# Optimization experiments

Hardware: AMD Instinct MI355X
Metric: run time of the kernel (lower is better)

## Reference

```python
import jax, jax.numpy as jnp
import numpy as np

D_MODEL = 1024
NUM_HEADS = 16
HEAD_DIM = D_MODEL // NUM_HEADS  # 64
THETA = 10000.0
B, S = 2, 2048


def setup_inputs() -> dict:
    key = jax.random.key(0)
    k1, k2, k3 = jax.random.split(key, 3)
    sigma_qkv = (2.0 / (D_MODEL + 3 * D_MODEL)) ** 0.5
    sigma_o = (2.0 / (D_MODEL + D_MODEL)) ** 0.5
    x = jax.random.normal(k1, (B, S, D_MODEL), dtype=jnp.float32)
    w_qkv = jax.random.normal(k2, (3 * D_MODEL, D_MODEL), dtype=jnp.float32) * sigma_qkv
    w_o = jax.random.normal(k3, (D_MODEL, D_MODEL), dtype=jnp.float32) * sigma_o
    token_positions = jnp.arange(S, dtype=jnp.int32)
    return {"x": x, "w_qkv": w_qkv, "w_o": w_o, "token_positions": token_positions, "mask": 1}


def _rope(t, pos):
    # t: (B, H, S, HEAD_DIM); pos: (S,) int
    ids = jnp.arange(HEAD_DIM // 2, dtype=jnp.float32)
    freqs = pos.astype(jnp.float32)[:, None] * (THETA ** (-2.0 * ids / HEAD_DIM))  # (S, HEAD_DIM/2)
    cos, sin = jnp.cos(freqs), jnp.sin(freqs)
    even, odd = t[..., 0::2], t[..., 1::2]
    r_even = even * cos - odd * sin
    r_odd = odd * cos + even * sin
    # interleave back to original layout
    return jnp.stack([r_even, r_odd], axis=-1).reshape(t.shape)


def reference(x, w_qkv, w_o, token_positions, mask):
    # fused QKV projection: Linear computes x @ W^T with W [out, in]
    qkv = x @ w_qkv.T  # (B, S, 3*D_MODEL)
    q, k, v = jnp.split(qkv, 3, axis=-1)

    def to_heads(t):
        return t.reshape(B, S, NUM_HEADS, HEAD_DIM).transpose(0, 2, 1, 3)  # (B, H, S, Dh)

    q, k, v = to_heads(q), to_heads(k), to_heads(v)
    q = _rope(q, token_positions)
    k = _rope(k, token_positions)

    scores = jnp.einsum('bhqd,bhkd->bhqk', q, k)
    if mask:  # causal: lower-triangular allowed
        causal = jnp.tril(jnp.ones((S, S), dtype=bool))
        scores = jnp.where(causal, scores, -jnp.inf)
    attn = jax.nn.softmax(scores * (HEAD_DIM ** -0.5), axis=-1)
    out = jnp.einsum('bhqk,bhkd->bhqd', attn, v)  # (B, H, S, Dh)
    out = out.transpose(0, 2, 1, 3).reshape(B, S, D_MODEL)
    return out @ w_o.T
```

## Files before the change

kernel.cpp:

```cpp
#include <hip/hip_runtime.h>
#include <hip/hip_bf16.h>
#include <math.h>

typedef __bf16 bf16_t;
typedef __bf16 bf16x8 __attribute__((ext_vector_type(8)));
typedef __bf16 bf16x4 __attribute__((ext_vector_type(4)));
typedef float  f32x4  __attribute__((ext_vector_type(4)));
typedef float  f32x16 __attribute__((ext_vector_type(16)));

#define D_MODEL 1024
#define NH      16
#define HD      64
#define BATCH   2
#define SEQ     2048
#define MROWS   (BATCH*SEQ)
#define QKVN    (3*D_MODEL)
#define FA_PAD  72
#define PADK    40
#define SCALE_LOG2E 0.18033688011112042f

__device__ __forceinline__ void async_cp16(const bf16_t* g, bf16_t* l) {
    __builtin_amdgcn_global_load_lds(
        (const __attribute__((address_space(1))) void*)g,
        (__attribute__((address_space(3))) void*)l,
        16, 0, 0);
}

__device__ __forceinline__ float fexp2(float x) {
    float r;
    asm("v_exp_f32 %0, %1" : "=v"(r) : "v"(x));
    return r;
}

__global__ void cvt_all(const float* __restrict__ x, const float* __restrict__ wq,
                        const float* __restrict__ wo,
                        bf16_t* __restrict__ xb, bf16_t* __restrict__ wqb,
                        bf16_t* __restrict__ wob) {
    const int nx = MROWS * D_MODEL, nq = QKVN * D_MODEL;
    int i = (blockIdx.x * blockDim.x + threadIdx.x) * 4;
    const float* s; bf16_t* d; int off;
    if (i < nx)           { s = x;  d = xb;  off = i; }
    else if (i < nx + nq) { s = wq; d = wqb; off = i - nx; }
    else                  { s = wo; d = wob; off = i - nx - nq; }
    float4 v = *(const float4*)(s + off);
    d[off]     = (bf16_t)v.x;
    d[off + 1] = (bf16_t)v.y;
    d[off + 2] = (bf16_t)v.z;
    d[off + 3] = (bf16_t)v.w;
}

template <typename OutT, int NI>
__global__ __launch_bounds__(256) void gemm_nt(const bf16_t* __restrict__ A,
                                               const bf16_t* __restrict__ Bm,
                                               OutT* __restrict__ C,
                                               int M, int N, int K) {
    __shared__ __align__(16) bf16_t As[128 * 32];
    __shared__ __align__(16) bf16_t Bs[NI * 32 * 32];
    const int tid  = threadIdx.x;
    const int w    = tid >> 6;
    const int lane = tid & 63;
    const int quad = lane >> 4;
    const int l16  = lane & 15;
    const int m0   = blockIdx.x * 128;
    const int n0   = blockIdx.y * (NI * 32);
    const int wm   = (w >> 1) * 64;
    const int wn   = (w & 1) * (NI * 16);

    f32x4 acc[4][NI];
    #pragma unroll
    for (int i = 0; i < 4; i++)
        #pragma unroll
        for (int j = 0; j < NI; j++)
            acc[i][j] = (f32x4){0.f, 0.f, 0.f, 0.f};

    const bf16_t* Ag0 = A  + (size_t)(m0 + (tid >> 2)) * K + (tid & 3) * 8;
    const bf16_t* Ag1 = Ag0 + (size_t)64 * K;
    const bf16_t* Bg0 = Bm + (size_t)(n0 + (tid >> 2)) * K + (tid & 3) * 8;
    const bf16_t* Bg1 = Bg0 + (size_t)64 * K;
    bf16_t* Al0 = &As[(size_t)tid * 8];
    bf16_t* Al1 = &As[((size_t)tid + 256) * 8];
    bf16_t* Bl0 = &Bs[(size_t)tid * 8];
    bf16_t* Bl1 = &Bs[((size_t)tid + 256) * 8];

    for (int k0 = 0; k0 < K; k0 += 32) {
        async_cp16(Ag0 + k0, Al0);
        async_cp16(Ag1 + k0, Al1);
        async_cp16(Bg0 + k0, Bl0);
        if (NI == 4) async_cp16(Bg1 + k0, Bl1);
        __syncthreads();

        bf16x8 af[4], bfr[NI];
        #pragma unroll
        for (int mi = 0; mi < 4; mi++)
            af[mi] = *(const bf16x8*)&As[(wm + mi * 16 + l16) * 32 + quad * 8];
        #pragma unroll
        for (int ni = 0; ni < NI; ni++)
            bfr[ni] = *(const bf16x8*)&Bs[(wn + ni * 16 + l16) * 32 + quad * 8];
        #pragma unroll
        for (int mi = 0; mi < 4; mi++)
            #pragma unroll
            for (int ni = 0; ni < NI; ni++)
                acc[mi][ni] = __builtin_amdgcn_mfma_f32_16x16x32_bf16(
                    af[mi], bfr[ni], acc[mi][ni], 0, 0, 0);
        __syncthreads();
    }

    #pragma unroll
    for (int mi = 0; mi < 4; mi++)
        #pragma unroll
        for (int ni = 0; ni < NI; ni++) {
            const int col = n0 + wn + ni * 16 + l16;
            #pragma unroll
            for (int r = 0; r < 4; r++) {
                const int row = m0 + wm + mi * 16 + quad * 4 + r;
                C[(size_t)row * N + col] = (OutT)acc[mi][ni][r];
            }
        }
}

__global__ __launch_bounds__(256) void rope_split(const bf16_t* __restrict__ qkv,
                                                  const int* __restrict__ pos,
                                                  bf16_t* __restrict__ Qh,
                                                  bf16_t* __restrict__ Kh,
                                                  bf16_t* __restrict__ VT) {
    __shared__ bf16_t vs[128][FA_PAD];
    const int tid   = threadIdx.x;
    const int s_loc = tid >> 1;
    const int half  = tid & 1;
    const int s0    = blockIdx.x * 128;
    const int bh    = blockIdx.y;
    const int b     = bh >> 4, h = bh & 15;
    const int s     = s0 + s_loc;

    const bf16_t* row = qkv + (size_t)(b * SEQ + s) * QKVN + h * HD + half * 32;

    bf16_t qbuf[32], kbuf[32], vbuf[32];
    #pragma unroll
    for (int j = 0; j < 4; j++) {
        *(bf16x8*)&qbuf[j * 8] = *(const bf16x8*)(row + j * 8);
        *(bf16x8*)&kbuf[j * 8] = *(const bf16x8*)(row + D_MODEL + j * 8);
        *(bf16x8*)&vbuf[j * 8] = *(const bf16x8*)(row + 2 * D_MODEL + j * 8);
    }

    const float pf = (float)pos[s];
    #pragma unroll
    for (int p = 0; p < 16; p++) {
        const int d2 = half * 16 + p;
        const float inv = __expf(-0.28782313662425575f * (float)d2);
        const float f = pf * inv;
        const float c = cosf(f), sn = sinf(f);
        float qe = (float)qbuf[2 * p], qo = (float)qbuf[2 * p + 1];
        float ke = (float)kbuf[2 * p], ko = (float)kbuf[2 * p + 1];
        qbuf[2 * p]     = (bf16_t)(qe * c - qo * sn);
        qbuf[2 * p + 1] = (bf16_t)(qo * c + qe * sn);
        kbuf[2 * p]     = (bf16_t)(ke * c - ko * sn);
        kbuf[2 * p + 1] = (bf16_t)(ko * c + ke * sn);
    }

    bf16_t* qdst = Qh + ((size_t)bh * SEQ + s) * HD + half * 32;
    bf16_t* kdst = Kh + ((size_t)bh * SEQ + s) * HD + half * 32;
    #pragma unroll
    for (int j = 0; j < 4; j++) {
        *(bf16x8*)(qdst + j * 8) = *(bf16x8*)&qbuf[j * 8];
        *(bf16x8*)(kdst + j * 8) = *(bf16x8*)&kbuf[j * 8];
        *(bf16x8*)&vs[s_loc][half * 32 + j * 8] = *(bf16x8*)&vbuf[j * 8];
    }
    __syncthreads();

    const int d  = tid >> 2;
    const int sc = tid & 3;
    bf16_t tmp[32];
    #pragma unroll
    for (int i = 0; i < 32; i++) tmp[i] = vs[sc * 32 + i][d];
    bf16_t* vdst = VT + ((size_t)bh * HD + d) * SEQ + s0 + sc * 32;
    #pragma unroll
    for (int j = 0; j < 4; j++)
        *(bf16x8*)(vdst + j * 8) = *(bf16x8*)&tmp[j * 8];
}

__global__ __launch_bounds__(256) void flash_attn(const bf16_t* __restrict__ Qh,
                                                  const bf16_t* __restrict__ Kh,
                                                  const bf16_t* __restrict__ VT,
                                                  bf16_t* __restrict__ AO) {
    __shared__ __align__(16) char smem[64 * FA_PAD * 2 * 2 + 4 * 32 * PADK * 2];
    bf16_t* Ks = (bf16_t*)smem;
    bf16_t* Vs = Ks + 64 * FA_PAD;
    bf16_t* pT = Vs + 64 * FA_PAD;

    const int tid  = threadIdx.x;
    const int w    = tid >> 6;
    const int lane = tid & 63;
    const int l31  = lane & 31;
    const int hi   = lane >> 5;
    const int qh   = w & 1;
    const int kh   = w >> 1;

    const int bid  = blockIdx.x;
    const int bh   = bid & 31;
    const int my_t = 31 - (bid >> 5);
    const int nkv  = my_t + 1;

    const bf16_t* Qb = Qh + (size_t)bh * SEQ * HD;
    const bf16_t* Kb = Kh + (size_t)bh * SEQ * HD;
    const bf16_t* Vb = VT + (size_t)bh * HD * SEQ;

    const int q0b = my_t * 64;
    const int qlo = q0b + qh * 32;
    const int qg  = qlo + l31;

    bf16x8 aq[4];
    #pragma unroll
    for (int ks = 0; ks < 4; ks++)
        aq[ks] = *(const bf16x8*)(Qb + (size_t)qg * HD + ks * 16 + hi * 8);

    const int srow = tid >> 3, scol = (tid & 7) * 8;
    const int lds0 = srow * FA_PAD + scol;
    const int lds1 = (srow + 32) * FA_PAD + scol;

    f32x16 o[2];
    #pragma unroll
    for (int dt = 0; dt < 2; dt++)
        #pragma unroll
        for (int i = 0; i < 16; i++) o[dt][i] = 0.f;
    float ls = 0.f;

    bf16x8 pK0 = *(const bf16x8*)(Kb + (size_t)srow * HD + scol);
    bf16x8 pK1 = *(const bf16x8*)(Kb + (size_t)(srow + 32) * HD + scol);
    bf16x8 pV0 = *(const bf16x8*)(Vb + (size_t)srow * SEQ + scol);
    bf16x8 pV1 = *(const bf16x8*)(Vb + (size_t)(srow + 32) * SEQ + scol);

    bf16_t* pb = &pT[(w * 32 + l31) * PADK];

    for (int kt = 0; kt < nkv; ++kt) {
        *(bf16x8*)&Ks[lds0] = pK0;
        *(bf16x8*)&Ks[lds1] = pK1;
        *(bf16x8*)&Vs[lds0] = pV0;
        *(bf16x8*)&Vs[lds1] = pV1;
        __syncthreads();

        if (kt + 1 < nkv) {
            const int kn = (kt + 1) * 64;
            pK0 = *(const bf16x8*)(Kb + (size_t)(kn + srow) * HD + scol);
            pK1 = *(const bf16x8*)(Kb + (size_t)(kn + srow + 32) * HD + scol);
            pV0 = *(const bf16x8*)(Vb + (size_t)srow * SEQ + kn + scol);
            pV1 = *(const bf16x8*)(Vb + (size_t)(srow + 32) * SEQ + kn + scol);
        }

        const int kvbw = kt * 64 + kh * 32;
        if (kvbw <= qlo + 31) {
            const bool full = (kvbw + 31 <= qlo);

            bf16x8 kb[4];
            #pragma unroll
            for (int ks = 0; ks < 4; ks++)
                kb[ks] = *(const bf16x8*)&Ks[(kh * 32 + l31) * FA_PAD + ks * 16 + hi * 8];
            f32x16 t;
            #pragma unroll
            for (int i = 0; i < 16; i++) t[i] = 0.f;
            #pragma unroll
            for (int ks = 0; ks < 4; ks++)
                t = __builtin_amdgcn_mfma_f32_32x32x16_bf16(kb[ks], aq[ks], t, 0, 0, 0);

            bf16x4 pk[4];
            #pragma unroll
            for (int r = 0; r < 16; r++) {
                float pv = fexp2(t[r] * SCALE_LOG2E);
                if (!full) {
                    const int kvg = kvbw + (r & 3) + 8 * (r >> 2) + 4 * hi;
                    if (kvg > qg) pv = 0.f;
                }
                ls += pv;
                pk[r >> 2][r & 3] = (bf16_t)pv;
            }
            #pragma unroll
            for (int g = 0; g < 4; g++)
                *(bf16x4*)&pb[8 * g + 4 * hi] = pk[g];

            bf16x8 pa0 = *(const bf16x8*)&pb[hi * 8];
            bf16x8 pa1 = *(const bf16x8*)&pb[16 + hi * 8];
            #pragma unroll
            for (int dt = 0; dt < 2; dt++) {
                const int vbase = (dt * 32 + l31) * FA_PAD + kh * 32 + hi * 8;
                bf16x8 vf0 = *(const bf16x8*)&Vs[vbase];
                bf16x8 vf1 = *(const bf16x8*)&Vs[vbase + 16];
                o[dt] = __builtin_amdgcn_mfma_f32_32x32x16_bf16(pa0, vf0, o[dt], 0, 0, 0);
                o[dt] = __builtin_amdgcn_mfma_f32_32x32x16_bf16(pa1, vf1, o[dt], 0, 0, 0);
            }
        }

        __syncthreads();
    }

    ls += __shfl_xor(ls, 32);
    float* mrgO = (float*)smem;
    float* lsp  = mrgO + 2 * 32 * 66;
    if (kh == 1) {
        #pragma unroll
        for (int r = 0; r < 16; r++) {
            const int qlc = (r & 3) + 8 * (r >> 2) + 4 * hi;
            #pragma unroll
            for (int dt = 0; dt < 2; dt++)
                mrgO[(qh * 32 + qlc) * 66 + dt * 32 + l31] = o[dt][r];
        }
        if (hi == 0) lsp[qh * 32 + l31] = ls;
    }
    __syncthreads();
    if (kh == 0) {
        const float lt = ls + lsp[qh * 32 + l31];
        const int b = bh >> 4, hh = bh & 15;
        #pragma unroll
        for (int r = 0; r < 16; r++) {
            const int qlc = (r & 3) + 8 * (r >> 2) + 4 * hi;
            const float li = 1.0f / __shfl(lt, qlc);
            const size_t row = (size_t)b * SEQ + q0b + qh * 32 + qlc;
            #pragma unroll
            for (int dt = 0; dt < 2; dt++) {
                const float v = o[dt][r] + mrgO[(qh * 32 + qlc) * 66 + dt * 32 + l31];
                AO[row * D_MODEL + hh * HD + dt * 32 + l31] = (bf16_t)(v * li);
            }
        }
    }
}

extern "C" void kernel_launch(void* const* d_in, const int* in_sizes, int n_in,
                              void* d_out, int out_size, void* d_ws, size_t ws_size,
                              hipStream_t stream) {
    const float* x     = (const float*)d_in[0];
    const float* w_qkv = (const float*)d_in[1];
    const float* w_o   = (const float*)d_in[2];
    const int*   tpos  = (const int*)d_in[3];
    float*       out   = (float*)d_out;

    char* ws = (char*)d_ws;
    bf16_t* xb  = (bf16_t*)(ws);
    bf16_t* wqb = (bf16_t*)(ws + 8388608);
    bf16_t* wob = (bf16_t*)(ws + 14680064);
    bf16_t* qkv = (bf16_t*)(ws + 16777216);
    bf16_t* Qh  = (bf16_t*)(ws + 41943040);
    bf16_t* Kh  = (bf16_t*)(ws + 50331648);
    bf16_t* VT  = (bf16_t*)(ws + 58720256);
    bf16_t* AO  = (bf16_t*)(ws + 67108864);

    cvt_all<<<8192, 256, 0, stream>>>(x, w_qkv, w_o, xb, wqb, wob);

    gemm_nt<bf16_t, 4><<<dim3(32, 24), 256, 0, stream>>>(xb, wqb, qkv, MROWS, QKVN, D_MODEL);

    rope_split<<<dim3(SEQ / 128, BATCH * NH), 256, 0, stream>>>(qkv, tpos, Qh, Kh, VT);

    flash_attn<<<1024, 256, 0, stream>>>(Qh, Kh, VT, AO);

    gemm_nt<float, 2><<<dim3(32, 16), 256, 0, stream>>>(AO, wob, out, MROWS, D_MODEL, D_MODEL);
}
```

Measured before the change: 193.8 us.

## Double-buffer K/V in LDS, keep P in registers via permlane swap, prescale Q

The flash attention kernel now uses two LDS buffers for K and V. Each iteration stores the next tile into the alternate buffer after compute, so one barrier per iteration replaces two. The probability tile no longer round-trips through LDS: it is packed with v_cvt_pk_bf16_f32 and rearranged with v_permlane32_swap into the MFMA A-operand layout in registers. The softmax scale times log2e is folded into Q during the RoPE pass, which removes a multiply per score but rounds the scaled Q to bf16.

```diff
diff --git a/kernel.cpp b/kernel.cpp
--- a/kernel.cpp
+++ b/kernel.cpp
@@ -16,7 +16,6 @@
 #define MROWS   (BATCH*SEQ)
 #define QKVN    (3*D_MODEL)
 #define FA_PAD  72
-#define PADK    40
 #define SCALE_LOG2E 0.18033688011112042f
 
 __device__ __forceinline__ void async_cp16(const bf16_t* g, bf16_t* l) {
@@ -29,6 +28,12 @@
 __device__ __forceinline__ float fexp2(float x) {
     float r;
     asm("v_exp_f32 %0, %1" : "=v"(r) : "v"(x));
+    return r;
+}
+
+__device__ __forceinline__ unsigned cvtpk(float lo, float hi_) {
+    unsigned r;
+    asm("v_cvt_pk_bf16_f32 %0, %1, %2" : "=v"(r) : "v"(lo), "v"(hi_));
     return r;
 }
 
@@ -151,8 +156,8 @@
         const float c = cosf(f), sn = sinf(f);
         float qe = (float)qbuf[2 * p], qo = (float)qbuf[2 * p + 1];
         float ke = (float)kbuf[2 * p], ko = (float)kbuf[2 * p + 1];
-        qbuf[2 * p]     = (bf16_t)(qe * c - qo * sn);
-        qbuf[2 * p + 1] = (bf16_t)(qo * c + qe * sn);
+        qbuf[2 * p]     = (bf16_t)((qe * c - qo * sn) * SCALE_LOG2E);
+        qbuf[2 * p + 1] = (bf16_t)((qo * c + qe * sn) * SCALE_LOG2E);
         kbuf[2 * p]     = (bf16_t)(ke * c - ko * sn);
         kbuf[2 * p + 1] = (bf16_t)(ko * c + ke * sn);
     }
@@ -182,10 +187,10 @@
                                                   const bf16_t* __restrict__ Kh,
                                                   const bf16_t* __restrict__ VT,
                                                   bf16_t* __restrict__ AO) {
-    __shared__ __align__(16) char smem[64 * FA_PAD * 2 * 2 + 4 * 32 * PADK * 2];
-    bf16_t* Ks = (bf16_t*)smem;
-    bf16_t* Vs = Ks + 64 * FA_PAD;
-    bf16_t* pT = Vs + 64 * FA_PAD;
+    __shared__ __align__(16) bf16_t smem[4 * 64 * FA_PAD];
+    bf16_t* Ks0 = smem;
+    bf16_t* Vs0 = smem + 2 * 64 * FA_PAD;
+    const int BUF = 64 * FA_PAD;
 
     const int tid  = threadIdx.x;
     const int w    = tid >> 6;
@@ -228,14 +233,13 @@
     bf16x8 pK1 = *(const bf16x8*)(Kb + (size_t)(srow + 32) * HD + scol);
     bf16x8 pV0 = *(const bf16x8*)(Vb + (size_t)srow * SEQ + scol);
     bf16x8 pV1 = *(const bf16x8*)(Vb + (size_t)(srow + 32) * SEQ + scol);
-
-    bf16_t* pb = &pT[(w * 32 + l31) * PADK];
+    *(bf16x8*)&Ks0[lds0] = pK0;
+    *(bf16x8*)&Ks0[lds1] = pK1;
+    *(bf16x8*)&Vs0[lds0] = pV0;
+    *(bf16x8*)&Vs0[lds1] = pV1;
 
     for (int kt = 0; kt < nkv; ++kt) {
-        *(bf16x8*)&Ks[lds0] = pK0;
-        *(bf16x8*)&Ks[lds1] = pK1;
-        *(bf16x8*)&Vs[lds0] = pV0;
-        *(bf16x8*)&Vs[lds1] = pV1;
+        const int cur = kt & 1;
         __syncthreads();
 
         if (kt + 1 < nkv) {
@@ -246,6 +250,8 @@
             pV1 = *(const bf16x8*)(Vb + (size_t)(srow + 32) * SEQ + kn + scol);
         }
 
+        const bf16_t* KsC = Ks0 + cur * BUF;
+        const bf16_t* VsC = Vs0 + cur * BUF;
         const int kvbw = kt * 64 + kh * 32;
         if (kvbw <= qlo + 31) {
             const bool full = (kvbw + 31 <= qlo);
@@ -253,7 +259,7 @@
             bf16x8 kb[4];
             #pragma unroll
             for (int ks = 0; ks < 4; ks++)
-                kb[ks] = *(const bf16x8*)&Ks[(kh * 32 + l31) * FA_PAD + ks * 16 + hi * 8];
+                kb[ks] = *(const bf16x8*)&KsC[(kh * 32 + l31) * FA_PAD + ks * 16 + hi * 8];
             f32x16 t;
             #pragma unroll
             for (int i = 0; i < 16; i++) t[i] = 0.f;
@@ -261,36 +267,62 @@
             for (int ks = 0; ks < 4; ks++)
                 t = __builtin_amdgcn_mfma_f32_32x32x16_bf16(kb[ks], aq[ks], t, 0, 0, 0);
 
-            bf16x4 pk[4];
+            float pv[16];
             #pragma unroll
             for (int r = 0; r < 16; r++) {
-                float pv = fexp2(t[r] * SCALE_LOG2E);
+                float p = fexp2(t[r]);
                 if (!full) {
                     const int kvg = kvbw + (r & 3) + 8 * (r >> 2) + 4 * hi;
-                    if (kvg > qg) pv = 0.f;
+                    if (kvg > qg) p = 0.f;
                 }
-                ls += pv;
-                pk[r >> 2][r & 3] = (bf16_t)pv;
-            }
-            #pragma unroll
-            for (int g = 0; g < 4; g++)
-                *(bf16x4*)&pb[8 * g + 4 * hi] = pk[g];
-
-            bf16x8 pa0 = *(const bf16x8*)&pb[hi * 8];
-            bf16x8 pa1 = *(const bf16x8*)&pb[16 + hi * 8];
+                pv[r] = p;
+            }
+            ls += ((((pv[0] + pv[1]) + (pv[2] + pv[3]))
+                  + ((pv[4] + pv[5]) + (pv[6] + pv[7])))
+                 + (((pv[8] + pv[9]) + (pv[10] + pv[11]))
+                  + ((pv[12] + pv[13]) + (pv[14] + pv[15]))));
+
+            union { unsigned u[4]; bf16x8 v; } pa0, pa1;
+            {
+                unsigned a0 = cvtpk(pv[0], pv[1]);
+                unsigned b0 = cvtpk(pv[4], pv[5]);
+                unsigned a1 = cvtpk(pv[2], pv[3]);
+                unsigned b1 = cvtpk(pv[6], pv[7]);
+                asm volatile("v_permlane32_swap_b32 %0, %1" : "+v"(a0), "+v"(b0));
+                asm volatile("v_permlane32_swap_b32 %0, %1" : "+v"(a1), "+v"(b1));
+                pa0.u[0] = a0; pa0.u[1] = a1; pa0.u[2] = b0; pa0.u[3] = b1;
+            }
+            {
+                unsigned a0 = cvtpk(pv[8], pv[9]);
+                unsigned b0 = cvtpk(pv[12], pv[13]);
+                unsigned a1 = cvtpk(pv[10], pv[11]);
+                unsigned b1 = cvtpk(pv[14], pv[15]);
+                asm volatile("v_permlane32_swap_b32 %0, %1" : "+v"(a0), "+v"(b0));
+                asm volatile("v_permlane32_swap_b32 %0, %1" : "+v"(a1), "+v"(b1));
+                pa1.u[0] = a0; pa1.u[1] = a1; pa1.u[2] = b0; pa1.u[3] = b1;
+            }
+
             #pragma unroll
             for (int dt = 0; dt < 2; dt++) {
                 const int vbase = (dt * 32 + l31) * FA_PAD + kh * 32 + hi * 8;
-                bf16x8 vf0 = *(const bf16x8*)&Vs[vbase];
-                bf16x8 vf1 = *(const bf16x8*)&Vs[vbase + 16];
-                o[dt] = __builtin_amdgcn_mfma_f32_32x32x16_bf16(pa0, vf0, o[dt], 0, 0, 0);
-                o[dt] = __builtin_amdgcn_mfma_f32_32x32x16_bf16(pa1, vf1, o[dt], 0, 0, 0);
-            }
-        }
-
-        __syncthreads();
-    }
-
+                bf16x8 vf0 = *(const bf16x8*)&VsC[vbase];
+                bf16x8 vf1 = *(const bf16x8*)&VsC[vbase + 16];
+                o[dt] = __builtin_amdgcn_mfma_f32_32x32x16_bf16(pa0.v, vf0, o[dt], 0, 0, 0);
+                o[dt] = __builtin_amdgcn_mfma_f32_32x32x16_bf16(pa1.v, vf1, o[dt], 0, 0, 0);
+            }
+        }
+
+        if (kt + 1 < nkv) {
+            bf16_t* KsN = Ks0 + (cur ^ 1) * BUF;
+            bf16_t* VsN = Vs0 + (cur ^ 1) * BUF;
+            *(bf16x8*)&KsN[lds0] = pK0;
+            *(bf16x8*)&KsN[lds1] = pK1;
+            *(bf16x8*)&VsN[lds0] = pV0;
+            *(bf16x8*)&VsN[lds1] = pV1;
+        }
+    }
+
+    __syncthreads();
     ls += __shfl_xor(ls, 32);
     float* mrgO = (float*)smem;
     float* lsp  = mrgO + 2 * 32 * 66;
```

Measured after the change: 192.2 us. No clear change (-0.8%).
